# Kernel optimization log

Measured on AMD Instinct MI355X. Metric: run time of the kernel, lower is better.

## Reference

```python
import jax, jax.numpy as jnp
import numpy as np

N_BATCH = 131072
N_MODES = 32
E_CONST = float(np.e)


def setup_inputs() -> dict:
    key = jax.random.key(0)
    k1, k2 = jax.random.split(key)
    phi = jax.random.normal(k1, (N_BATCH, N_MODES), dtype=jnp.float32)
    Gamma = jax.random.uniform(k2, (N_MODES, N_MODES), dtype=jnp.float32)
    w = jnp.zeros((N_MODES,), dtype=jnp.float32)
    return {"phi": phi, "Gamma": Gamma, "w": w}


def reference(phi, Gamma, w):
    # train=True path: mode_min starts at +inf, so mode_min = per-mode batch min
    M = Gamma.shape[0]
    mode_min = jnp.min(phi, axis=0)                      # [M]
    phic = phi - mode_min[None, :] + E_CONST             # [N, M]
    phic = jnp.maximum(phic, E_CONST)                    # clamp: phi[phi<e] = e

    # symmetric gamma lookup: g(i,j) = Gamma[min(i,j), max(i,j)]
    idx = jnp.arange(M)
    G = jnp.where(idx[:, None] < idx[None, :], Gamma, Gamma.T)  # [M, M]

    # off-diagonal partial energies: phi_i^g * phi_j^(1-g)
    pe_off = phic[:, :, None] ** G[None, :, :] * phic[:, None, :] ** (1.0 - G[None, :, :])  # [N,M,M]
    off_mask = 1.0 - jnp.eye(M, dtype=phic.dtype)
    # diagonal term: (1 + w_i) * phi_i
    mode_energies = jnp.sum(pe_off * off_mask, axis=-1) + (1.0 + w)[None, :] * phic  # [N, M]

    t = 1.0 / np.sqrt(M)
    logits = jax.nn.log_softmax(-t * mode_energies, axis=-1)
    alphas = jnp.exp(logits)
    return alphas, logits
```

## Files before the change

### kernel.cpp

```cpp
#include <hip/hip_runtime.h>
#include <math.h>

#define NB 131072
#define NM 32
#define EC 2.7182818284590452f
#define TS 0.17677669529663687f
#define L2E 1.4426950408889634f
#define LN2F 0.6931471805599453f


#if __has_builtin(__builtin_amdgcn_exp2f)
__device__ __forceinline__ float fexp2(float x) { return __builtin_amdgcn_exp2f(x); }
#else
__device__ __forceinline__ float fexp2(float x) { return exp2f(x); }
#endif
#if __has_builtin(__builtin_amdgcn_logf)
__device__ __forceinline__ float flog2(float x) { return __builtin_amdgcn_logf(x); }
#else
__device__ __forceinline__ float flog2(float x) { return __log2f(x); }
#endif

__global__ __launch_bounds__(256) void k_min(const float* __restrict__ phi,
                                             float* __restrict__ ws) {
    __shared__ float sm[1024];
    const int tid = threadIdx.x;
    const int g = blockIdx.x * 256 + tid;
    const float4* __restrict__ p4 = (const float4*)phi;
    float4 m = p4[g];
    #pragma unroll
    for (int k = 1; k < 16; ++k) {
        float4 v = p4[g + k * 65536];
        m.x = fminf(m.x, v.x); m.y = fminf(m.y, v.y);
        m.z = fminf(m.z, v.z); m.w = fminf(m.w, v.w);
    }
    sm[tid * 4 + 0] = m.x; sm[tid * 4 + 1] = m.y;
    sm[tid * 4 + 2] = m.z; sm[tid * 4 + 3] = m.w;
    __syncthreads();
    #pragma unroll
    for (int s = 128; s >= 8; s >>= 1) {
        if (tid < s) {
            sm[tid * 4 + 0] = fminf(sm[tid * 4 + 0], sm[(tid + s) * 4 + 0]);
            sm[tid * 4 + 1] = fminf(sm[tid * 4 + 1], sm[(tid + s) * 4 + 1]);
            sm[tid * 4 + 2] = fminf(sm[tid * 4 + 2], sm[(tid + s) * 4 + 2]);
            sm[tid * 4 + 3] = fminf(sm[tid * 4 + 3], sm[(tid + s) * 4 + 3]);
        }
        __syncthreads();
    }
    if (tid < 8) {
        #pragma unroll
        for (int s2 = 0; s2 < 4; ++s2)
            ws[2048 + blockIdx.x * 32 + tid * 4 + s2] = sm[tid * 4 + s2];
    }
}

__global__ __launch_bounds__(64) void k_prep(const float* __restrict__ Gamma,
                                             float* __restrict__ ws) {
    __shared__ float sm[64];
    const int tid = threadIdx.x;
    const int c = tid & 31, h = tid >> 5;
    float m = INFINITY;
    #pragma unroll 8
    for (int b = h * 128; b < (h + 1) * 128; ++b)
        m = fminf(m, ws[2048 + b * 32 + c]);
    sm[tid] = m;
    __syncthreads();
    if (tid < 32) ws[1024 + tid] = fminf(sm[tid], sm[tid + 32]) - EC;
    #pragma unroll
    for (int k = 0; k < 16; ++k) {
        int idx = tid + 64 * k;
        int i = idx >> 5, j = idx & 31;
        int lo = min(i, j), hi = i + j - lo;
        ws[idx] = Gamma[lo * 32 + hi];
    }
}

__global__ __launch_bounds__(64, 2) void k_main(const float* __restrict__ phi,
                                                const float* __restrict__ w,
                                                const float* __restrict__ ws,
                                                float* __restrict__ out) {
    __shared__ float sL[32 * 65];
    __shared__ float sX[32 * 65];
    const int lane = threadIdx.x;
    const size_t row = (size_t)blockIdx.x * 64 + lane;
    const float* __restrict__ pr = phi + row * NM;
    const float* __restrict__ mme = ws + 1024;

    float L[32];
    #pragma unroll
    for (int k = 0; k < 8; ++k) {
        float4 v = ((const float4*)pr)[k];
        float a0 = fmaxf(v.x - mme[4 * k + 0], EC);
        float a1 = fmaxf(v.y - mme[4 * k + 1], EC);
        float a2 = fmaxf(v.z - mme[4 * k + 2], EC);
        float a3 = fmaxf(v.w - mme[4 * k + 3], EC);
        L[4 * k + 0] = flog2(a0); L[4 * k + 1] = flog2(a1);
        L[4 * k + 2] = flog2(a2); L[4 * k + 3] = flog2(a3);
    }
    #pragma unroll
    for (int j = 0; j < 32; ++j) sL[j * 65 + lane] = L[j];
    __syncthreads();

    for (int i = 0; i < 32; ++i) {
        const float Li = sL[i * 65 + lane];
        const float* __restrict__ g = ws + i * 32;
        float acc0 = 0.f, acc1 = 0.f, acc2 = 0.f, acc3 = 0.f;
        #pragma unroll
        for (int j = 0; j < 32; j += 4) {
            acc0 += fexp2(fmaf(g[j + 0], Li - L[j + 0], L[j + 0]));
            acc1 += fexp2(fmaf(g[j + 1], Li - L[j + 1], L[j + 1]));
            acc2 += fexp2(fmaf(g[j + 2], Li - L[j + 2], L[j + 2]));
            acc3 += fexp2(fmaf(g[j + 3], Li - L[j + 3], L[j + 3]));
        }
        const float e = ((acc0 + acc1) + (acc2 + acc3)) + w[i] * fexp2(Li);
        sX[i * 65 + lane] = -TS * e;
    }
    __syncthreads();

    float xs[32];
    #pragma unroll
    for (int i = 0; i < 32; ++i) xs[i] = sX[i * 65 + lane];
    float m = xs[0];
    #pragma unroll
    for (int i = 1; i < 32; ++i) m = fmaxf(m, xs[i]);
    float p[32];
    float s = 0.f;
    #pragma unroll
    for (int i = 0; i < 32; ++i) { p[i] = fexp2((xs[i] - m) * L2E); s += p[i]; }
    const float inv = 1.0f / s;
    const float lns = flog2(s) * LN2F;

    float* __restrict__ oa = out + row * NM;
    float* __restrict__ ol = out + (size_t)NB * NM + row * NM;
    #pragma unroll
    for (int k = 0; k < 8; ++k) {
        float4 a4 = { p[4 * k + 0] * inv, p[4 * k + 1] * inv,
                      p[4 * k + 2] * inv, p[4 * k + 3] * inv };
        float4 l4 = { (xs[4 * k + 0] - m) - lns, (xs[4 * k + 1] - m) - lns,
                      (xs[4 * k + 2] - m) - lns, (xs[4 * k + 3] - m) - lns };
        ((float4*)oa)[k] = a4;
        ((float4*)ol)[k] = l4;
    }
}

extern "C" void kernel_launch(void* const* d_in, const int* in_sizes, int n_in,
                              void* d_out, int out_size, void* d_ws, size_t ws_size,
                              hipStream_t stream) {
    (void)in_sizes; (void)n_in; (void)out_size; (void)ws_size;
    const float* phi   = (const float*)d_in[0];
    const float* Gamma = (const float*)d_in[1];
    const float* w     = (const float*)d_in[2];
    float* out = (float*)d_out;
    float* wsf = (float*)d_ws;

    k_min<<<256, 256, 0, stream>>>(phi, wsf);
    k_prep<<<1, 64, 0, stream>>>(Gamma, wsf);
    k_main<<<2048, 64, 0, stream>>>(phi, w, wsf, out);
}
```

Measured before the change: 126.6 us.

## Fully unroll main energy loop in registers and widen blocks to 256 threads

The main kernel no longer stages per-row log values and energies through shared memory. It fully unrolls the outer i loop so L[i] and xs[i] are indexed at compile time and stay in registers, which removes both __syncthreads and the LDS traffic. Blocks grow from 64 to 256 threads, the prep kernel spreads its min reduction across 256 threads, and the diagonal term reuses the clamped phi value instead of recomputing exp2(log2). In exchange, the 32x32 unrolled body raises register pressure and code size, which may lower occupancy.

```diff
diff --git a/kernel.cpp b/kernel.cpp
--- a/kernel.cpp
+++ b/kernel.cpp
@@ -53,72 +53,70 @@
     }
 }
 
-__global__ __launch_bounds__(64) void k_prep(const float* __restrict__ Gamma,
-                                             float* __restrict__ ws) {
-    __shared__ float sm[64];
+__global__ __launch_bounds__(256) void k_prep(const float* __restrict__ Gamma,
+                                              float* __restrict__ ws) {
+    __shared__ float sm[256];
     const int tid = threadIdx.x;
     const int c = tid & 31, h = tid >> 5;
     float m = INFINITY;
-    #pragma unroll 8
-    for (int b = h * 128; b < (h + 1) * 128; ++b)
-        m = fminf(m, ws[2048 + b * 32 + c]);
+    #pragma unroll
+    for (int b = 0; b < 32; ++b)
+        m = fminf(m, ws[2048 + (h * 32 + b) * 32 + c]);
     sm[tid] = m;
     __syncthreads();
-    if (tid < 32) ws[1024 + tid] = fminf(sm[tid], sm[tid + 32]) - EC;
+    if (tid < 32) {
+        float mm = sm[tid];
+        #pragma unroll
+        for (int g2 = 1; g2 < 8; ++g2) mm = fminf(mm, sm[g2 * 32 + tid]);
+        ws[1024 + tid] = mm - EC;
+    }
     #pragma unroll
-    for (int k = 0; k < 16; ++k) {
-        int idx = tid + 64 * k;
+    for (int k = 0; k < 4; ++k) {
+        int idx = tid + 256 * k;
         int i = idx >> 5, j = idx & 31;
         int lo = min(i, j), hi = i + j - lo;
         ws[idx] = Gamma[lo * 32 + hi];
     }
 }
 
-__global__ __launch_bounds__(64, 2) void k_main(const float* __restrict__ phi,
-                                                const float* __restrict__ w,
-                                                const float* __restrict__ ws,
-                                                float* __restrict__ out) {
-    __shared__ float sL[32 * 65];
-    __shared__ float sX[32 * 65];
-    const int lane = threadIdx.x;
-    const size_t row = (size_t)blockIdx.x * 64 + lane;
+__global__ __launch_bounds__(256) void k_main(const float* __restrict__ phi,
+                                              const float* __restrict__ w,
+                                              const float* __restrict__ ws,
+                                              float* __restrict__ out) {
+    const int tid = threadIdx.x;
+    const size_t row = (size_t)blockIdx.x * 256 + tid;
     const float* __restrict__ pr = phi + row * NM;
     const float* __restrict__ mme = ws + 1024;
 
-    float L[32];
+    float L[32], ph[32];
     #pragma unroll
     for (int k = 0; k < 8; ++k) {
         float4 v = ((const float4*)pr)[k];
-        float a0 = fmaxf(v.x - mme[4 * k + 0], EC);
-        float a1 = fmaxf(v.y - mme[4 * k + 1], EC);
-        float a2 = fmaxf(v.z - mme[4 * k + 2], EC);
-        float a3 = fmaxf(v.w - mme[4 * k + 3], EC);
-        L[4 * k + 0] = flog2(a0); L[4 * k + 1] = flog2(a1);
-        L[4 * k + 2] = flog2(a2); L[4 * k + 3] = flog2(a3);
+        ph[4 * k + 0] = fmaxf(v.x - mme[4 * k + 0], EC);
+        ph[4 * k + 1] = fmaxf(v.y - mme[4 * k + 1], EC);
+        ph[4 * k + 2] = fmaxf(v.z - mme[4 * k + 2], EC);
+        ph[4 * k + 3] = fmaxf(v.w - mme[4 * k + 3], EC);
+        L[4 * k + 0] = flog2(ph[4 * k + 0]);
+        L[4 * k + 1] = flog2(ph[4 * k + 1]);
+        L[4 * k + 2] = flog2(ph[4 * k + 2]);
+        L[4 * k + 3] = flog2(ph[4 * k + 3]);
     }
+
+    float xs[32];
     #pragma unroll
-    for (int j = 0; j < 32; ++j) sL[j * 65 + lane] = L[j];
-    __syncthreads();
-
     for (int i = 0; i < 32; ++i) {
-        const float Li = sL[i * 65 + lane];
-        const float* __restrict__ g = ws + i * 32;
+        const float Li = L[i];
         float acc0 = 0.f, acc1 = 0.f, acc2 = 0.f, acc3 = 0.f;
         #pragma unroll
         for (int j = 0; j < 32; j += 4) {
-            acc0 += fexp2(fmaf(g[j + 0], Li - L[j + 0], L[j + 0]));
-            acc1 += fexp2(fmaf(g[j + 1], Li - L[j + 1], L[j + 1]));
-            acc2 += fexp2(fmaf(g[j + 2], Li - L[j + 2], L[j + 2]));
-            acc3 += fexp2(fmaf(g[j + 3], Li - L[j + 3], L[j + 3]));
+            acc0 += fexp2(fmaf(ws[i * 32 + j + 0], Li - L[j + 0], L[j + 0]));
+            acc1 += fexp2(fmaf(ws[i * 32 + j + 1], Li - L[j + 1], L[j + 1]));
+            acc2 += fexp2(fmaf(ws[i * 32 + j + 2], Li - L[j + 2], L[j + 2]));
+            acc3 += fexp2(fmaf(ws[i * 32 + j + 3], Li - L[j + 3], L[j + 3]));
         }
-        const float e = ((acc0 + acc1) + (acc2 + acc3)) + w[i] * fexp2(Li);
-        sX[i * 65 + lane] = -TS * e;
+        xs[i] = -TS * ((((acc0 + acc1) + (acc2 + acc3)) + w[i] * ph[i]));
     }
-    __syncthreads();
 
-    float xs[32];
-    #pragma unroll
-    for (int i = 0; i < 32; ++i) xs[i] = sX[i * 65 + lane];
     float m = xs[0];
     #pragma unroll
     for (int i = 1; i < 32; ++i) m = fmaxf(m, xs[i]);
@@ -153,6 +151,6 @@
     float* wsf = (float*)d_ws;
 
     k_min<<<256, 256, 0, stream>>>(phi, wsf);
-    k_prep<<<1, 64, 0, stream>>>(Gamma, wsf);
-    k_main<<<2048, 64, 0, stream>>>(phi, w, wsf, out);
+    k_prep<<<1, 256, 0, stream>>>(Gamma, wsf);
+    k_main<<<512, 256, 0, stream>>>(phi, w, wsf, out);
 }
```

Result: faster. 109.9 us (-13.2%).
